# Performance work log

Hardware: AMD Instinct MI355X
Metric: run time of the kernel (lower is better)

Reference implementation:

```python
import jax, jax.numpy as jnp
import numpy as np

DIM = 256
NUM_HEADS = 4
KEY_DIM = 16
ATTN_RATIO = 2
D = ATTN_RATIO * KEY_DIM  # 32
WS = 7
QKV_DIM = NUM_HEADS * KEY_DIM * 2 + NUM_HEADS * D  # 256
SCALE = KEY_DIM ** -0.5


def setup_inputs() -> dict:
    key = jax.random.key(0)
    k1, k2, k3 = jax.random.split(key, 3)
    x = jax.random.normal(k1, (32, DIM, 112, 112), jnp.float32)
    # Linear weights stored as [in, out] so y = x @ W + b (same math as torch's x @ W.T)
    Wqkv = jax.random.normal(k2, (DIM, QKV_DIM), jnp.float32) * 0.05
    bqkv = jnp.zeros((QKV_DIM,), jnp.float32)
    Wproj = jax.random.normal(k3, (NUM_HEADS * D, DIM), jnp.float32) * 0.05
    bproj = jnp.zeros((DIM,), jnp.float32)
    return {"x": x, "Wqkv": Wqkv, "bqkv": bqkv, "Wproj": Wproj, "bproj": bproj}


def reference(x, Wqkv, bqkv, Wproj, bproj):
    B, C, H, W = x.shape
    ws = WS
    pad_h = (ws - H % ws) % ws
    pad_w = (ws - W % ws) % ws
    xp = jnp.pad(x, ((0, 0), (0, 0), (0, pad_h), (0, pad_w)))
    Hp, Wp = H + pad_h, W + pad_w
    nwh, nww = Hp // ws, Wp // ws
    N = ws * ws  # tokens per window (49)
    # window partition: (B, C, nwh, ws, nww, ws) -> (B*nwh*nww, N, C)
    xw = xp.reshape(B, C, nwh, ws, nww, ws).transpose(0, 2, 4, 3, 5, 1)
    xw = xw.reshape(B * nwh * nww, N, C)
    # tiny multi-head attention within each window
    qkv = xw @ Wqkv + bqkv  # [Bw, N, QKV_DIM]
    qt = NUM_HEADS * KEY_DIM
    q = qkv[:, :, :qt].reshape(-1, N, NUM_HEADS, KEY_DIM).transpose(0, 2, 1, 3)
    k = qkv[:, :, qt:2 * qt].reshape(-1, N, NUM_HEADS, KEY_DIM).transpose(0, 2, 1, 3)
    v = qkv[:, :, 2 * qt:].reshape(-1, N, NUM_HEADS, D).transpose(0, 2, 1, 3)
    attn = jax.nn.softmax(jnp.einsum('bhnd,bhmd->bhnm', q, k) * SCALE, axis=-1)
    o = jnp.einsum('bhnm,bhmd->bhnd', attn, v)  # [Bw, H, N, D]
    o = o.transpose(0, 2, 1, 3).reshape(-1, N, NUM_HEADS * D)
    o = o @ Wproj + bproj  # [Bw, N, C]
    # window merge: reverse of the partition
    o = o.reshape(B, nwh, nww, ws, ws, C).transpose(0, 5, 1, 3, 2, 4)
    o = o.reshape(B, C, Hp, Wp)
    return o[:, :, :H, :W]
```

## Files before the change

### kernel.cpp

```cpp
#include <hip/hip_runtime.h>
#include <hip/hip_bf16.h>


typedef short bf16x8 __attribute__((ext_vector_type(8)));
typedef float f32x4 __attribute__((ext_vector_type(4)));

static __device__ __forceinline__ unsigned short cvt1(float f) {
    __hip_bfloat16 h = __float2bfloat16(f);
    unsigned short u; __builtin_memcpy(&u, &h, 2); return u;
}
static __device__ __forceinline__ unsigned int cvt2(float a, float b) {
    float2 t; t.x = a; t.y = b;
    __hip_bfloat162 h = __float22bfloat162_rn(t);
    unsigned int u; __builtin_memcpy(&u, &h, 4); return u;
}
static __device__ __forceinline__ float bf2f(unsigned int hs) {
    return __uint_as_float(hs << 16);
}

#define PROJ_OFF 65536

__global__ void prep_weights(const float* __restrict__ Wqkv,
                             const float* __restrict__ Wproj,
                             unsigned short* __restrict__ ws) {
    int tid = blockIdx.x * 256 + threadIdx.x;
    if (tid < 8192) {
        int lane = tid & 63, f = tid >> 6;
        int kt = f & 7, nt = f >> 3;
        int kbase = kt * 32 + (lane >> 4) * 8;
        int col = nt * 16 + (lane & 15);
        uint4 u;
        u.x = cvt2(Wqkv[(kbase + 0) * 256 + col], Wqkv[(kbase + 1) * 256 + col]);
        u.y = cvt2(Wqkv[(kbase + 2) * 256 + col], Wqkv[(kbase + 3) * 256 + col]);
        u.z = cvt2(Wqkv[(kbase + 4) * 256 + col], Wqkv[(kbase + 5) * 256 + col]);
        u.w = cvt2(Wqkv[(kbase + 6) * 256 + col], Wqkv[(kbase + 7) * 256 + col]);
        *reinterpret_cast<uint4*>(&ws[tid * 8]) = u;
    } else if (tid < 12288) {
        int i2 = tid - 8192;
        int lane = i2 & 63, f = i2 >> 6;
        int kt = f & 3, nt = f >> 2;
        int kbase = kt * 32 + (lane >> 4) * 8;
        int col = nt * 16 + (lane & 15);
        uint4 u;
        u.x = cvt2(Wproj[(kbase + 0) * 256 + col], Wproj[(kbase + 1) * 256 + col]);
        u.y = cvt2(Wproj[(kbase + 2) * 256 + col], Wproj[(kbase + 3) * 256 + col]);
        u.z = cvt2(Wproj[(kbase + 4) * 256 + col], Wproj[(kbase + 5) * 256 + col]);
        u.w = cvt2(Wproj[(kbase + 6) * 256 + col], Wproj[(kbase + 7) * 256 + col]);
        *reinterpret_cast<uint4*>(&ws[PROJ_OFF + i2 * 8]) = u;
    }
}


__global__ __launch_bounds__(256, 3) void win_attn(
    const float* __restrict__ x,
    const unsigned short* __restrict__ wf,
    const float* __restrict__ bqkv,
    const float* __restrict__ bproj,
    float* __restrict__ out)
{
    __shared__ __align__(16) unsigned short A[16384];
    __shared__ __align__(16) unsigned short B[8192];

    const int tid  = threadIdx.x;
    const int lane = tid & 63;
    const int wave = tid >> 6;
    const int lr   = lane & 15;
    const int kg   = lane >> 4;

    const int bid = (int)blockIdx.x;
    const int L   = (bid & 7) * 1024 + (bid >> 3);
    const int b   = L >> 8;
    const int rem = L & 255;
    const int h0 = (rem >> 4) * 7;
    const int w0 = (rem & 15) * 7;
    const int xwin = (b * 256) * 12544 + h0 * 112 + w0;

    float bqv[4], bpv[4];
    #pragma unroll
    for (int nn = 0; nn < 4; ++nn) {
        bqv[nn] = bqkv[wave * 64 + nn * 16 + lr];
        bpv[nn] = bproj[wave * 64 + nn * 16 + lr];
    }

    for (int i = tid; i < 15 * 128; i += 256)
        reinterpret_cast<unsigned int*>(A)[49 * 128 + i] = 0u;

    if (lane < 49) {
        const int lb = xwin + (lane / 7) * 112 + (lane % 7);
        #pragma unroll 8
        for (int it = 0; it < 32; ++it) {
            const int c0 = wave * 64 + it * 2;
            const float v0 = x[lb + c0 * 12544];
            const float v1 = x[lb + (c0 + 1) * 12544];
            const int e = lane * 256 + (((c0 >> 3) ^ (lane & 7)) << 3) + (c0 & 7);
            *reinterpret_cast<unsigned int*>(&A[e]) = cvt2(v0, v1);
        }
    }
    __syncthreads();

    f32x4 acc[4][4];
    #pragma unroll
    for (int m = 0; m < 4; ++m)
        #pragma unroll
        for (int nn = 0; nn < 4; ++nn)
            acc[m][nn] = f32x4{0.f, 0.f, 0.f, 0.f};

    #pragma unroll
    for (int kt = 0; kt < 8; ++kt) {
        bf16x8 a[4], bw[4];
        #pragma unroll
        for (int m = 0; m < 4; ++m) {
            const int row = lr + 16 * m;
            const int ch  = (kt * 4 + kg) ^ (row & 7);
            a[m] = *reinterpret_cast<const bf16x8*>(&A[row * 256 + ch * 8]);
        }
        #pragma unroll
        for (int nn = 0; nn < 4; ++nn) {
            const int nt = wave * 4 + nn;
            bw[nn] = *reinterpret_cast<const bf16x8*>(&wf[((nt * 8 + kt) * 64 + lane) * 8]);
        }
        #pragma unroll
        for (int m = 0; m < 4; ++m)
            #pragma unroll
            for (int nn = 0; nn < 4; ++nn)
                acc[m][nn] = __builtin_amdgcn_mfma_f32_16x16x32_bf16(a[m], bw[nn], acc[m][nn], 0, 0, 0);
    }
    __syncthreads();

    #pragma unroll
    for (int nn = 0; nn < 4; ++nn) {
        const int colg = wave * 64 + nn * 16 + lr;
        #pragma unroll
        for (int m = 0; m < 4; ++m)
            #pragma unroll
            for (int r = 0; r < 4; ++r) {
                const int row = kg * 4 + r + 16 * m;
                const unsigned short hv = cvt1(acc[m][nn][r] + bqv[nn]);
                if (wave < 2) {
                    B[row * 128 + (((colg >> 3) ^ (row & 7)) << 3) + (colg & 7)] = hv;
                } else {
                    const int vc = colg - 128;
                    const int hh = vc >> 5, d = vc & 31;
                    A[8192 + hh * 2048 + d * 64 + (((row >> 3) ^ (d & 7)) << 3) + (row & 7)] = hv;
                }
            }
    }
    __syncthreads();

    const int h = wave;
    f32x4 s[4][4];
    {
        bf16x8 qf[4], kf[4];
        const bf16x8 zf = {0, 0, 0, 0, 0, 0, 0, 0};
        #pragma unroll
        for (int m = 0; m < 4; ++m) {
            if (lane < 32) {
                const int row = lr + 16 * m;
                const int col = h * 16 + kg * 8;
                qf[m] = *reinterpret_cast<const bf16x8*>(&B[row * 128 + (((col >> 3) ^ (row & 7)) << 3)]);
            } else qf[m] = zf;
        }
        #pragma unroll
        for (int nt = 0; nt < 4; ++nt) {
            if (lane < 32) {
                const int row = lr + 16 * nt;
                const int col = 64 + h * 16 + kg * 8;
                kf[nt] = *reinterpret_cast<const bf16x8*>(&B[row * 128 + (((col >> 3) ^ (row & 7)) << 3)]);
            } else kf[nt] = zf;
        }
        #pragma unroll
        for (int m = 0; m < 4; ++m)
            #pragma unroll
            for (int nt = 0; nt < 4; ++nt) {
                f32x4 z = f32x4{0.f, 0.f, 0.f, 0.f};
                s[m][nt] = __builtin_amdgcn_mfma_f32_16x16x32_bf16(qf[m], kf[nt], z, 0, 0, 0);
            }
    }

    bf16x8 vb[2][2];
    #pragma unroll
    for (int kt = 0; kt < 2; ++kt)
        #pragma unroll
        for (int nt = 0; nt < 2; ++nt) {
            const int d = lr + 16 * nt;
            const int ch = (kt * 4 + kg) ^ (d & 7);
            vb[kt][nt] = *reinterpret_cast<const bf16x8*>(&A[8192 + h * 2048 + d * 64 + ch * 8]);
        }

    f32x4 oacc[4][2];
    #pragma unroll
    for (int m = 0; m < 4; ++m) {
        oacc[m][0] = f32x4{0.f, 0.f, 0.f, 0.f};
        oacc[m][1] = f32x4{0.f, 0.f, 0.f, 0.f};
    }
    float rs[4][4];
    const bool v3 = (lr == 0);

    #pragma unroll
    for (int mh = 0; mh < 2; ++mh) {
        #pragma unroll
        for (int m2 = 0; m2 < 2; ++m2) {
            const int m = mh * 2 + m2;
            float mx[4], sum[4];
            #pragma unroll
            for (int r = 0; r < 4; ++r) {
                const float a0 = fmaxf(s[m][0][r], s[m][1][r]);
                const float a1 = v3 ? fmaxf(s[m][2][r], s[m][3][r]) : s[m][2][r];
                mx[r] = fmaxf(a0, a1);
            }
            #pragma unroll
            for (int d = 1; d <= 8; d <<= 1)
                #pragma unroll
                for (int r = 0; r < 4; ++r)
                    mx[r] = fmaxf(mx[r], __shfl_xor(mx[r], d, 64));
            #pragma unroll
            for (int r = 0; r < 4; ++r) sum[r] = 0.f;
            #pragma unroll
            for (int nt = 0; nt < 4; ++nt)
                #pragma unroll
                for (int r = 0; r < 4; ++r) {
                    const float e = (nt == 3 && !v3) ? 0.f
                                  : __expf((s[m][nt][r] - mx[r]) * 0.25f);
                    s[m][nt][r] = e;
                    sum[r] += e;
                }
            #pragma unroll
            for (int d = 1; d <= 8; d <<= 1)
                #pragma unroll
                for (int r = 0; r < 4; ++r)
                    sum[r] += __shfl_xor(sum[r], d, 64);
            #pragma unroll
            for (int r = 0; r < 4; ++r) rs[m][r] = __builtin_amdgcn_rcpf(sum[r]);
            #pragma unroll
            for (int nt = 0; nt < 4; ++nt)
                #pragma unroll
                for (int r = 0; r < 4; ++r) {
                    const int rw = kg * 4 + r + 16 * m2;
                    const int col = lr + 16 * nt;
                    A[h * 2048 + rw * 64 + (((col >> 3) ^ (rw & 7)) << 3) + (col & 7)] =
                        cvt1(s[m][nt][r]);
                }
        }
        #pragma unroll
        for (int kt = 0; kt < 2; ++kt) {
            bf16x8 pa[2];
            #pragma unroll
            for (int m2 = 0; m2 < 2; ++m2) {
                const int rw = lr + 16 * m2;
                const int ch = (kt * 4 + kg) ^ (rw & 7);
                pa[m2] = *reinterpret_cast<const bf16x8*>(&A[h * 2048 + rw * 64 + ch * 8]);
            }
            #pragma unroll
            for (int m2 = 0; m2 < 2; ++m2)
                #pragma unroll
                for (int nt = 0; nt < 2; ++nt)
                    oacc[mh * 2 + m2][nt] =
                        __builtin_amdgcn_mfma_f32_16x16x32_bf16(pa[m2], vb[kt][nt], oacc[mh * 2 + m2][nt], 0, 0, 0);
        }
    }
    #pragma unroll
    for (int m = 0; m < 4; ++m)
        #pragma unroll
        for (int nt = 0; nt < 2; ++nt)
            #pragma unroll
            for (int r = 0; r < 4; ++r)
                oacc[m][nt][r] *= rs[m][r];

    __syncthreads();

    #pragma unroll
    for (int m = 0; m < 4; ++m)
        #pragma unroll
        for (int nt = 0; nt < 2; ++nt)
            #pragma unroll
            for (int r = 0; r < 4; ++r) {
                const int row = kg * 4 + r + 16 * m;
                const int col = h * 32 + nt * 16 + lr;
                B[row * 128 + (((col >> 3) ^ (row & 7)) << 3) + (col & 7)] = cvt1(oacc[m][nt][r]);
            }
    __syncthreads();

    f32x4 pc[4][4];
    #pragma unroll
    for (int m = 0; m < 4; ++m)
        #pragma unroll
        for (int nn = 0; nn < 4; ++nn)
            pc[m][nn] = f32x4{0.f, 0.f, 0.f, 0.f};

    #pragma unroll
    for (int kt = 0; kt < 4; ++kt) {
        bf16x8 a[4], bw[4];
        #pragma unroll
        for (int m = 0; m < 4; ++m) {
            const int row = lr + 16 * m;
            const int ch = (kt * 4 + kg) ^ (row & 7);
            a[m] = *reinterpret_cast<const bf16x8*>(&B[row * 128 + ch * 8]);
        }
        #pragma unroll
        for (int nn = 0; nn < 4; ++nn) {
            const int nt = wave * 4 + nn;
            bw[nn] = *reinterpret_cast<const bf16x8*>(&wf[PROJ_OFF + ((nt * 4 + kt) * 64 + lane) * 8]);
        }
        #pragma unroll
        for (int m = 0; m < 4; ++m)
            #pragma unroll
            for (int nn = 0; nn < 4; ++nn)
                pc[m][nn] = __builtin_amdgcn_mfma_f32_16x16x32_bf16(a[m], bw[nn], pc[m][nn], 0, 0, 0);
    }

    #pragma unroll
    for (int nn = 0; nn < 4; ++nn) {
        const int colg = wave * 64 + nn * 16 + lr;
        #pragma unroll
        for (int m = 0; m < 4; ++m)
            #pragma unroll
            for (int r = 0; r < 4; ++r) {
                const int row = kg * 4 + r + 16 * m;
                A[row * 256 + (((colg >> 3) ^ (row & 7)) << 3) + (colg & 7)] = cvt1(pc[m][nn][r] + bpv[nn]);
            }
    }
    __syncthreads();

    if (lane < 49) {
        const int lb = xwin + (lane / 7) * 112 + (lane % 7);
        #pragma unroll 8
        for (int it = 0; it < 32; ++it) {
            const int c0 = wave * 64 + it * 2;
            const int e = lane * 256 + (((c0 >> 3) ^ (lane & 7)) << 3) + (c0 & 7);
            const unsigned int pk = *reinterpret_cast<const unsigned int*>(&A[e]);
            out[lb + c0 * 12544] = bf2f(pk & 0xffffu);
            out[lb + (c0 + 1) * 12544] = bf2f(pk >> 16);
        }
    }
}

extern "C" void kernel_launch(void* const* d_in, const int* in_sizes, int n_in,
                              void* d_out, int out_size, void* d_ws, size_t ws_size,
                              hipStream_t stream) {
    const float* x     = (const float*)d_in[0];
    const float* Wqkv  = (const float*)d_in[1];
    const float* bqkv  = (const float*)d_in[2];
    const float* Wproj = (const float*)d_in[3];
    const float* bproj = (const float*)d_in[4];
    unsigned short* wf = (unsigned short*)d_ws;

    prep_weights<<<48, 256, 0, stream>>>(Wqkv, Wproj, wf);
    win_attn<<<8192, 256, 0, stream>>>(x, wf, bqkv, bproj, (float*)d_out);
}
```

Measured before the change: 440.8 us.

## Shrink LDS, drop softmax max-subtraction, compute row sums via MFMA

Moves the Q/K staging into the A buffer and swaps the 16KB B buffer for an 8KB per-head P buffer. Shared memory per block drops, which lets launch bounds rise from 3 to 4 blocks per CU. The softmax no longer subtracts the row max: it applies exp2 directly with a folded scale and gets row sums from an MFMA against a ones vector, removing the shuffle reductions. It also widens the global load/store packing to 4 channels and replaces the final block barrier with a wave barrier. Skipping the max subtraction risks overflow for large logits, and the tighter register budget may cause spills.

```diff
diff --git a/kernel.cpp b/kernel.cpp
--- a/kernel.cpp
+++ b/kernel.cpp
@@ -51,7 +51,7 @@
 }
 
 
-__global__ __launch_bounds__(256, 3) void win_attn(
+__global__ __launch_bounds__(256, 4) void win_attn(
     const float* __restrict__ x,
     const unsigned short* __restrict__ wf,
     const float* __restrict__ bqkv,
@@ -59,7 +59,7 @@
     float* __restrict__ out)
 {
     __shared__ __align__(16) unsigned short A[16384];
-    __shared__ __align__(16) unsigned short B[8192];
+    __shared__ __align__(16) unsigned short Pb[4096];
 
     const int tid  = threadIdx.x;
     const int lane = tid & 63;
@@ -87,13 +87,16 @@
 
     if (lane < 49) {
         const int lb = xwin + (lane / 7) * 112 + (lane % 7);
-        #pragma unroll 8
-        for (int it = 0; it < 32; ++it) {
-            const int c0 = wave * 64 + it * 2;
-            const float v0 = x[lb + c0 * 12544];
+        #pragma unroll 4
+        for (int it = 0; it < 16; ++it) {
+            const int c0 = wave * 64 + it * 4;
+            const float v0 = x[lb + (c0 + 0) * 12544];
             const float v1 = x[lb + (c0 + 1) * 12544];
+            const float v2 = x[lb + (c0 + 2) * 12544];
+            const float v3 = x[lb + (c0 + 3) * 12544];
+            uint2 pk; pk.x = cvt2(v0, v1); pk.y = cvt2(v2, v3);
             const int e = lane * 256 + (((c0 >> 3) ^ (lane & 7)) << 3) + (c0 & 7);
-            *reinterpret_cast<unsigned int*>(&A[e]) = cvt2(v0, v1);
+            *reinterpret_cast<uint2*>(&A[e]) = pk;
         }
     }
     __syncthreads();
@@ -137,7 +140,8 @@
                 const int row = kg * 4 + r + 16 * m;
                 const unsigned short hv = cvt1(acc[m][nn][r] + bqv[nn]);
                 if (wave < 2) {
-                    B[row * 128 + (((colg >> 3) ^ (row & 7)) << 3) + (colg & 7)] = hv;
+                    const int c = colg & 63;
+                    A[(wave << 12) + row * 64 + (((c >> 3) ^ (row & 7)) << 3) + (c & 7)] = hv;
                 } else {
                     const int vc = colg - 128;
                     const int hh = vc >> 5, d = vc & 31;
@@ -148,36 +152,17 @@
     __syncthreads();
 
     const int h = wave;
-    f32x4 s[4][4];
-    {
-        bf16x8 qf[4], kf[4];
-        const bf16x8 zf = {0, 0, 0, 0, 0, 0, 0, 0};
-        #pragma unroll
-        for (int m = 0; m < 4; ++m) {
-            if (lane < 32) {
-                const int row = lr + 16 * m;
-                const int col = h * 16 + kg * 8;
-                qf[m] = *reinterpret_cast<const bf16x8*>(&B[row * 128 + (((col >> 3) ^ (row & 7)) << 3)]);
-            } else qf[m] = zf;
-        }
-        #pragma unroll
-        for (int nt = 0; nt < 4; ++nt) {
-            if (lane < 32) {
-                const int row = lr + 16 * nt;
-                const int col = 64 + h * 16 + kg * 8;
-                kf[nt] = *reinterpret_cast<const bf16x8*>(&B[row * 128 + (((col >> 3) ^ (row & 7)) << 3)]);
-            } else kf[nt] = zf;
-        }
-        #pragma unroll
-        for (int m = 0; m < 4; ++m)
-            #pragma unroll
-            for (int nt = 0; nt < 4; ++nt) {
-                f32x4 z = f32x4{0.f, 0.f, 0.f, 0.f};
-                s[m][nt] = __builtin_amdgcn_mfma_f32_16x16x32_bf16(qf[m], kf[nt], z, 0, 0, 0);
-            }
-    }
-
-    bf16x8 vb[2][2];
+
+    bf16x8 kf[4], vb[2][2];
+    const bf16x8 zf = {0, 0, 0, 0, 0, 0, 0, 0};
+    #pragma unroll
+    for (int nt = 0; nt < 4; ++nt) {
+        if (lane < 32) {
+            const int row = lr + 16 * nt;
+            kf[nt] = *reinterpret_cast<const bf16x8*>(
+                &A[4096 + row * 64 + (((h * 2 + kg) ^ (row & 7)) << 3)]);
+        } else kf[nt] = zf;
+    }
     #pragma unroll
     for (int kt = 0; kt < 2; ++kt)
         #pragma unroll
@@ -186,98 +171,72 @@
             const int ch = (kt * 4 + kg) ^ (d & 7);
             vb[kt][nt] = *reinterpret_cast<const bf16x8*>(&A[8192 + h * 2048 + d * 64 + ch * 8]);
         }
-
-    f32x4 oacc[4][2];
+    const bf16x8 ones = {(short)16256, (short)16256, (short)16256, (short)16256,
+                         (short)16256, (short)16256, (short)16256, (short)16256};
+
+    f32x4 oacc[4][2], sacc[4];
     #pragma unroll
     for (int m = 0; m < 4; ++m) {
         oacc[m][0] = f32x4{0.f, 0.f, 0.f, 0.f};
         oacc[m][1] = f32x4{0.f, 0.f, 0.f, 0.f};
-    }
-    float rs[4][4];
+        sacc[m]    = f32x4{0.f, 0.f, 0.f, 0.f};
+    }
     const bool v3 = (lr == 0);
-
-    #pragma unroll
-    for (int mh = 0; mh < 2; ++mh) {
-        #pragma unroll
-        for (int m2 = 0; m2 < 2; ++m2) {
-            const int m = mh * 2 + m2;
-            float mx[4], sum[4];
+    const float C = 0.25f * 1.44269504f;
+
+    #pragma unroll
+    for (int m = 0; m < 4; ++m) {
+        bf16x8 qf;
+        if (lane < 32) {
+            const int row = lr + 16 * m;
+            qf = *reinterpret_cast<const bf16x8*>(
+                &A[row * 64 + (((h * 2 + kg) ^ (row & 7)) << 3)]);
+        } else qf = zf;
+
+        f32x4 s[4];
+        #pragma unroll
+        for (int nt = 0; nt < 4; ++nt) {
+            f32x4 z = f32x4{0.f, 0.f, 0.f, 0.f};
+            s[nt] = __builtin_amdgcn_mfma_f32_16x16x32_bf16(qf, kf[nt], z, 0, 0, 0);
+        }
+
+        #pragma unroll
+        for (int nt = 0; nt < 4; ++nt)
             #pragma unroll
             for (int r = 0; r < 4; ++r) {
-                const float a0 = fmaxf(s[m][0][r], s[m][1][r]);
-                const float a1 = v3 ? fmaxf(s[m][2][r], s[m][3][r]) : s[m][2][r];
-                mx[r] = fmaxf(a0, a1);
+                const float e = (nt == 3 && !v3) ? 0.f : __builtin_amdgcn_exp2f(s[nt][r] * C);
+                const int rw = kg * 4 + r;
+                const int col = lr + 16 * nt;
+                Pb[h * 1024 + rw * 64 + (((col >> 3) ^ (rw & 7)) << 3) + (col & 7)] = cvt1(e);
             }
-            #pragma unroll
-            for (int d = 1; d <= 8; d <<= 1)
-                #pragma unroll
-                for (int r = 0; r < 4; ++r)
-                    mx[r] = fmaxf(mx[r], __shfl_xor(mx[r], d, 64));
-            #pragma unroll
-            for (int r = 0; r < 4; ++r) sum[r] = 0.f;
-            #pragma unroll
-            for (int nt = 0; nt < 4; ++nt)
-                #pragma unroll
-                for (int r = 0; r < 4; ++r) {
-                    const float e = (nt == 3 && !v3) ? 0.f
-                                  : __expf((s[m][nt][r] - mx[r]) * 0.25f);
-                    s[m][nt][r] = e;
-                    sum[r] += e;
-                }
-            #pragma unroll
-            for (int d = 1; d <= 8; d <<= 1)
-                #pragma unroll
-                for (int r = 0; r < 4; ++r)
-                    sum[r] += __shfl_xor(sum[r], d, 64);
-            #pragma unroll
-            for (int r = 0; r < 4; ++r) rs[m][r] = __builtin_amdgcn_rcpf(sum[r]);
-            #pragma unroll
-            for (int nt = 0; nt < 4; ++nt)
-                #pragma unroll
-                for (int r = 0; r < 4; ++r) {
-                    const int rw = kg * 4 + r + 16 * m2;
-                    const int col = lr + 16 * nt;
-                    A[h * 2048 + rw * 64 + (((col >> 3) ^ (rw & 7)) << 3) + (col & 7)] =
-                        cvt1(s[m][nt][r]);
-                }
-        }
+
         #pragma unroll
         for (int kt = 0; kt < 2; ++kt) {
-            bf16x8 pa[2];
-            #pragma unroll
-            for (int m2 = 0; m2 < 2; ++m2) {
-                const int rw = lr + 16 * m2;
-                const int ch = (kt * 4 + kg) ^ (rw & 7);
-                pa[m2] = *reinterpret_cast<const bf16x8*>(&A[h * 2048 + rw * 64 + ch * 8]);
-            }
-            #pragma unroll
-            for (int m2 = 0; m2 < 2; ++m2)
-                #pragma unroll
-                for (int nt = 0; nt < 2; ++nt)
-                    oacc[mh * 2 + m2][nt] =
-                        __builtin_amdgcn_mfma_f32_16x16x32_bf16(pa[m2], vb[kt][nt], oacc[mh * 2 + m2][nt], 0, 0, 0);
-        }
-    }
-    #pragma unroll
-    for (int m = 0; m < 4; ++m)
-        #pragma unroll
-        for (int nt = 0; nt < 2; ++nt)
-            #pragma unroll
-            for (int r = 0; r < 4; ++r)
-                oacc[m][nt][r] *= rs[m][r];
-
-    __syncthreads();
-
-    #pragma unroll
-    for (int m = 0; m < 4; ++m)
+            const int ch = (kt * 4 + kg) ^ (lr & 7);
+            const bf16x8 pa = *reinterpret_cast<const bf16x8*>(&Pb[h * 1024 + lr * 64 + ch * 8]);
+            oacc[m][0] = __builtin_amdgcn_mfma_f32_16x16x32_bf16(pa, vb[kt][0], oacc[m][0], 0, 0, 0);
+            oacc[m][1] = __builtin_amdgcn_mfma_f32_16x16x32_bf16(pa, vb[kt][1], oacc[m][1], 0, 0, 0);
+            sacc[m]    = __builtin_amdgcn_mfma_f32_16x16x32_bf16(pa, ones,      sacc[m],    0, 0, 0);
+        }
+    }
+
+    __syncthreads();
+
+    #pragma unroll
+    for (int m = 0; m < 4; ++m) {
+        f32x4 rs;
+        #pragma unroll
+        for (int r = 0; r < 4; ++r) rs[r] = __builtin_amdgcn_rcpf(sacc[m][r]);
         #pragma unroll
         for (int nt = 0; nt < 2; ++nt)
             #pragma unroll
             for (int r = 0; r < 4; ++r) {
                 const int row = kg * 4 + r + 16 * m;
                 const int col = h * 32 + nt * 16 + lr;
-                B[row * 128 + (((col >> 3) ^ (row & 7)) << 3) + (col & 7)] = cvt1(oacc[m][nt][r]);
+                A[row * 128 + (((col >> 3) ^ (row & 7)) << 3) + (col & 7)] =
+                    cvt1(oacc[m][nt][r] * rs[r]);
             }
+    }
     __syncthreads();
 
     f32x4 pc[4][4];
@@ -294,7 +253,7 @@
         for (int m = 0; m < 4; ++m) {
             const int row = lr + 16 * m;
             const int ch = (kt * 4 + kg) ^ (row & 7);
-            a[m] = *reinterpret_cast<const bf16x8*>(&B[row * 128 + ch * 8]);
+            a[m] = *reinterpret_cast<const bf16x8*>(&A[row * 128 + ch * 8]);
         }
         #pragma unroll
         for (int nn = 0; nn < 4; ++nn) {
@@ -307,6 +266,7 @@
             for (int nn = 0; nn < 4; ++nn)
                 pc[m][nn] = __builtin_amdgcn_mfma_f32_16x16x32_bf16(a[m], bw[nn], pc[m][nn], 0, 0, 0);
     }
+    __syncthreads();
 
     #pragma unroll
     for (int nn = 0; nn < 4; ++nn) {
@@ -319,17 +279,19 @@
                 A[row * 256 + (((colg >> 3) ^ (row & 7)) << 3) + (colg & 7)] = cvt1(pc[m][nn][r] + bpv[nn]);
             }
     }
-    __syncthreads();
+    __builtin_amdgcn_wave_barrier();
 
     if (lane < 49) {
         const int lb = xwin + (lane / 7) * 112 + (lane % 7);
-        #pragma unroll 8
-        for (int it = 0; it < 32; ++it) {
-            const int c0 = wave * 64 + it * 2;
+        #pragma unroll 4
+        for (int it = 0; it < 16; ++it) {
+            const int c0 = wave * 64 + it * 4;
             const int e = lane * 256 + (((c0 >> 3) ^ (lane & 7)) << 3) + (c0 & 7);
-            const unsigned int pk = *reinterpret_cast<const unsigned int*>(&A[e]);
-            out[lb + c0 * 12544] = bf2f(pk & 0xffffu);
-            out[lb + (c0 + 1) * 12544] = bf2f(pk >> 16);
+            const uint2 pk = *reinterpret_cast<const uint2*>(&A[e]);
+            out[lb + (c0 + 0) * 12544] = bf2f(pk.x & 0xffffu);
+            out[lb + (c0 + 1) * 12544] = bf2f(pk.x >> 16);
+            out[lb + (c0 + 2) * 12544] = bf2f(pk.y & 0xffffu);
+            out[lb + (c0 + 3) * 12544] = bf2f(pk.y >> 16);
         }
     }
 }
```

New measurement: 520.1 us. 1.18x slower.
